# Optimization experiments

Measured on AMD Instinct MI355X. Metric: run time of the kernel, lower is better.

The kernel has to match this reference:

```python
import jax, jax.numpy as jnp
import numpy as np
from jax.ops import segment_sum

N_NODES = 100000
N_HEDGES = 20000
N_EDGES = 800000
N_TYPES = 2
IN_DIM = 64
HID = 64
OUT_DIM = 64


def setup_inputs() -> dict:
    key = jax.random.key(0)
    ks = jax.random.split(key, 16)
    inp = {
        "x": jax.random.normal(ks[0], (N_NODES, IN_DIM), jnp.float32),
        "h_prev": jax.random.normal(ks[1], (N_NODES, HID), jnp.float32),
        "node_idx": jax.random.randint(ks[2], (N_EDGES,), 0, N_NODES),
        "hedge_idx": jax.random.randint(ks[3], (N_EDGES,), 0, N_HEDGES),
        "edge_attr": jax.random.randint(ks[4], (N_EDGES,), 0, N_TYPES),
        "W_conv": jax.random.normal(ks[5], (N_TYPES, IN_DIM, HID), jnp.float32) * 0.05,
        "b_conv": jax.random.normal(ks[6], (N_TYPES, HID), jnp.float32) * 0.05,
        "W_mix": jax.random.normal(ks[7], (N_TYPES * HID, HID), jnp.float32) * 0.05,
        "b_mix": jax.random.normal(ks[8], (HID,), jnp.float32) * 0.05,
        "W_ih": jax.random.normal(ks[9], (HID, 3 * HID), jnp.float32) * 0.05,
        "W_hh": jax.random.normal(ks[10], (HID, 3 * HID), jnp.float32) * 0.05,
        "b_ih": jax.random.normal(ks[11], (3 * HID,), jnp.float32) * 0.05,
        "b_hh": jax.random.normal(ks[12], (3 * HID,), jnp.float32) * 0.05,
        "W_ro": jax.random.normal(ks[13], (HID, OUT_DIM), jnp.float32) * 0.05,
        "b_ro": jax.random.normal(ks[14], (OUT_DIM,), jnp.float32) * 0.05,
    }
    return inp


def _hypergraph_conv(x, node_idx, hedge_idx, mask, W, b):
    # PyG HypergraphConv (no attention): out = D^{-1} H B^{-1} H^T (x W) + b,
    # restricted to incidences where mask==1 (per edge type).
    xl = x @ W  # [N, hid]
    D = segment_sum(mask, node_idx, num_segments=N_NODES)       # node degree
    B = segment_sum(mask, hedge_idx, num_segments=N_HEDGES)     # hyperedge degree
    Dinv = jnp.where(D > 0, 1.0 / D, 0.0)
    Binv = jnp.where(B > 0, 1.0 / B, 0.0)
    # node -> hyperedge aggregation, scaled by B^{-1}
    ef = segment_sum(mask[:, None] * xl[node_idx], hedge_idx, num_segments=N_HEDGES)
    ef = ef * Binv[:, None]
    # hyperedge -> node aggregation, scaled by D^{-1}
    no = segment_sum(mask[:, None] * ef[hedge_idx], node_idx, num_segments=N_NODES)
    no = no * Dinv[:, None]
    return no + b


def reference(x, h_prev, node_idx, hedge_idx, edge_attr,
              W_conv, b_conv, W_mix, b_mix,
              W_ih, W_hh, b_ih, b_hh, W_ro, b_ro):
    outs = []
    for t in range(N_TYPES):
        mask = (edge_attr == t).astype(x.dtype)
        outs.append(_hypergraph_conv(x, node_idx, hedge_idx, mask, W_conv[t], b_conv[t]))
    h = jax.nn.relu(jnp.concatenate(outs, axis=1) @ W_mix + b_mix)  # [N, hid]
    # torch GRUCell: gates ordered (reset, update, new)
    gi = h @ W_ih + b_ih
    gh = h_prev @ W_hh + b_hh
    gi_r, gi_z, gi_n = jnp.split(gi, 3, axis=1)
    gh_r, gh_z, gh_n = jnp.split(gh, 3, axis=1)
    r = jax.nn.sigmoid(gi_r + gh_r)
    z = jax.nn.sigmoid(gi_z + gh_z)
    n = jnp.tanh(gi_n + r * gh_n)
    h_next = (1.0 - z) * n + z * h_prev
    out = (h_next @ W_ro + b_ro)[:, :3]
    return (h_next, out)
```

## Files before the change

kernel.cpp:

```cpp
#include <hip/hip_runtime.h>
#include <hip/hip_bf16.h>

#define N_NODES 100000
#define N_HEDGES 20000
#define N_EDGES 800000
#define HSEG (2 * N_HEDGES)
#define NSEG (2 * N_NODES)
#define MSEG (HSEG + NSEG)

#define EPB 4096
#define NBLK_A ((N_EDGES + EPB - 1) / EPB)
#define NHB 313
#define NBUCK 704
#define TOTB (NBUCK * NBLK_A)
#define SCANB ((TOTB + 2047) / 2048)
#define RKCAP 8192

#define CAST_BLOCKS (N_NODES * 64 / 8 / 256)
#define PACK_BLOCKS 16

#define MIX_PK  (4 * 4 * 64 * 8)
#define GRU_PK  (2 * 2 * 12 * 64 * 8)

typedef __hip_bfloat16 bf16;
typedef __attribute__((ext_vector_type(8))) short bf16x8;
typedef __attribute__((ext_vector_type(4))) float f32x4;

__device__ __forceinline__ bf16 f2b(float v) { return __float2bfloat16(v); }
__device__ __forceinline__ short f2s(float v) {
    bf16 b = __float2bfloat16(v);
    return *reinterpret_cast<short*>(&b);
}
__device__ __forceinline__ uint pk2(float a, float b) {
    return (uint)(unsigned short)f2s(a) | ((uint)(unsigned short)f2s(b) << 16);
}
__device__ __forceinline__ bf16x8 pack8(float4 a, float4 b) {
    bf16x8 r = {f2s(a.x), f2s(a.y), f2s(a.z), f2s(a.w),
                f2s(b.x), f2s(b.y), f2s(b.z), f2s(b.w)};
    return r;
}
__device__ __forceinline__ float fast_sigmoid(float x) {
    return __builtin_amdgcn_rcpf(1.f + __expf(-x));
}
__device__ __forceinline__ float fast_tanh(float x) {
    return 1.f - 2.f * __builtin_amdgcn_rcpf(1.f + __expf(2.f * x));
}

__global__ __launch_bounds__(256) void k_front(
    const int* __restrict__ node_idx, const int* __restrict__ hedge_idx,
    const int* __restrict__ attr, uint* __restrict__ rk12,
    int* __restrict__ bcnt,
    const float* __restrict__ x, bf16* __restrict__ xb,
    const float* __restrict__ Wc, const float* __restrict__ Wm,
    const float* __restrict__ bc_g, const float* __restrict__ bm,
    const float* __restrict__ Wih, const float* __restrict__ Whh,
    bf16* __restrict__ gru_pk, bf16* __restrict__ mixf_pk,
    float* __restrict__ bfused) {
    __shared__ int bc[NBUCK];
    int b = blockIdx.x;
    int tid = threadIdx.x;
    if (b < NBLK_A) {
        for (int i = tid; i < NBUCK; i += 256) bc[i] = 0;
        __syncthreads();
        int e0 = b * EPB;
        for (int it = 0; it < EPB / 256; ++it) {
            int e = e0 + it * 256 + tid;
            if (e < N_EDGES) {
                int t = attr[e];
                int s1 = t * N_HEDGES + hedge_idx[e];
                int s2 = HSEG + t * N_NODES + node_idx[e];
                int b1 = s1 >> 7;
                int b2 = NHB + ((s2 - HSEG) >> 9);
                int r1 = atomicAdd(&bc[b1], 1);
                int r2 = atomicAdd(&bc[b2], 1);
                rk12[e] = (uint)(r1 & 0xFFFF) | ((uint)r2 << 16);
            }
        }
        __syncthreads();
        for (int i = tid; i < NBUCK; i += 256) bcnt[i * NBLK_A + b] = bc[i];
    } else if (b < NBLK_A + CAST_BLOCKS) {
        size_t i = ((size_t)(b - NBLK_A) * 256 + tid) * 8;
        const float* xp = x + i;
        float4 a = *(const float4*)xp;
        float4 bb = *(const float4*)(xp + 4);
        *(bf16x8*)(xb + i) = pack8(a, bb);
    } else {
        int idx = (b - NBLK_A - CAST_BLOCKS) * 256 + tid;
        int stride = PACK_BLOCKS * 256;
        for (int i = idx; i < GRU_PK; i += stride) {
            int j = i & 7;
            int r = i >> 3;
            int ln = r & 63;
            int r2i = r >> 6;
            int ct = r2i % 12;
            int r3 = r2i / 12;
            int kt = r3 & 1;
            int mat = r3 >> 1;
            int k = kt * 32 + ((ln >> 4) << 3) + j;
            int n = ct * 16 + (ln & 15);
            float v = mat == 0 ? Wih[k * 192 + n] : Whh[k * 192 + n];
            gru_pk[i] = f2b(v);
        }
        for (int i = idx; i < MIX_PK; i += stride) {
            int j = i & 7, ln = (i >> 3) & 63, r2i = i >> 9;
            int ct = r2i & 3, kt = r2i >> 2;
            int k = kt * 32 + ((ln >> 4) << 3) + j;
            int n = ct * 16 + (ln & 15);
            int t = k >> 6, kk = k & 63;
            float s = 0.f;
            for (int q = 0; q < 64; ++q)
                s += Wc[((size_t)t * 64 + kk) * 64 + q] * Wm[(size_t)(t * 64 + q) * 64 + n];
            mixf_pk[i] = f2b(s);
        }
        for (int i = idx; i < 64; i += stride) {
            float s = bm[i];
            for (int q = 0; q < 64; ++q)
                s += bc_g[q] * Wm[(size_t)q * 64 + i] + bc_g[64 + q] * Wm[(size_t)(64 + q) * 64 + i];
            bfused[i] = s;
        }
    }
}

__global__ __launch_bounds__(256) void k_scan1(const int* __restrict__ cnt,
                                               int* __restrict__ off,
                                               int* __restrict__ bsum) {
    __shared__ int s[256];
    int base = blockIdx.x * 2048 + threadIdx.x * 8;
    int v[8];
    int tsum = 0;
#pragma unroll
    for (int j = 0; j < 8; ++j) {
        int g = base + j;
        v[j] = (g < TOTB) ? cnt[g] : 0;
        tsum += v[j];
    }
    s[threadIdx.x] = tsum;
    __syncthreads();
    for (int o = 1; o < 256; o <<= 1) {
        int t = (threadIdx.x >= o) ? s[threadIdx.x - o] : 0;
        __syncthreads();
        s[threadIdx.x] += t;
        __syncthreads();
    }
    int run = s[threadIdx.x] - tsum;
#pragma unroll
    for (int j = 0; j < 8; ++j) {
        int g = base + j;
        if (g < TOTB) off[g] = run;
        run += v[j];
    }
    if (threadIdx.x == 255) bsum[blockIdx.x] = s[255];
}

__global__ __launch_bounds__(1024) void k_scan2(int* __restrict__ bsum) {
    __shared__ int s[1024];
    int tid = threadIdx.x;
    int v = (tid < SCANB) ? bsum[tid] : 0;
    s[tid] = v;
    __syncthreads();
    for (int o = 1; o < 1024; o <<= 1) {
        int t = (tid >= o) ? s[tid - o] : 0;
        __syncthreads();
        s[tid] += t;
        __syncthreads();
    }
    if (tid < SCANB) bsum[tid] = s[tid] - v;
}

__global__ __launch_bounds__(256) void k_scan3(int* __restrict__ off,
                                               const int* __restrict__ bsum) {
    int base = blockIdx.x * 2048 + threadIdx.x * 8;
    int add = bsum[blockIdx.x];
#pragma unroll
    for (int j = 0; j < 8; ++j) {
        int g = base + j;
        if (g < TOTB) off[g] += add;
    }
    if (blockIdx.x == 0 && threadIdx.x == 0) off[TOTB] = 2 * N_EDGES;
}

__global__ __launch_bounds__(256) void k_bscatter(const int* __restrict__ node_idx,
                                                  const int* __restrict__ hedge_idx,
                                                  const int* __restrict__ attr,
                                                  const uint* __restrict__ rk12,
                                                  const int* __restrict__ bbase,
                                                  int2* __restrict__ pairs) {
    int b = blockIdx.x, tid = threadIdx.x;
    int e0 = b * EPB;
    for (int it = 0; it < EPB / 256; ++it) {
        int e = e0 + it * 256 + tid;
        if (e < N_EDGES) {
            int t = attr[e], n = node_idx[e], h = hedge_idx[e];
            int s1 = t * N_HEDGES + h;
            int s2 = HSEG + t * N_NODES + n;
            int b1 = s1 >> 7;
            int b2 = NHB + ((s2 - HSEG) >> 9);
            uint rk = rk12[e];
            int p1 = bbase[b1 * NBLK_A + b] + (int)(rk & 0xFFFF);
            int p2 = bbase[b2 * NBLK_A + b] + (int)(rk >> 16);
            pairs[p1] = make_int2(s1, n);
            pairs[p2] = make_int2(s2, t * N_HEDGES + h);
        }
    }
}

__global__ __launch_bounds__(256) void k_bfinal(const int* __restrict__ bbase,
                                                const int2* __restrict__ pairs,
                                                int* __restrict__ off,
                                                int* __restrict__ sortedAll) {
    __shared__ int scnt[512];
    __shared__ int exs[512];
    __shared__ int ssum[256];
    __shared__ unsigned short rk[RKCAP];
    int bucket = blockIdx.x, tid = threadIdx.x;
    int seg_first, nseg;
    if (bucket < NHB) {
        seg_first = bucket << 7;
        nseg = min(128, HSEG - seg_first);
    } else {
        int bi = bucket - NHB;
        seg_first = HSEG + (bi << 9);
        nseg = min(512, MSEG - seg_first);
    }
    int bstart = bbase[bucket * NBLK_A];
    int bend = bbase[(bucket + 1) * NBLK_A];
    for (int i = tid; i < 512; i += 256) scnt[i] = 0;
    __syncthreads();
    for (int i = bstart + tid; i < bend; i += 256) {
        int li = i - bstart;
        int key = pairs[i].x;
        int r = atomicAdd(&scnt[key - seg_first], 1);
        if (li < RKCAP) rk[li] = (unsigned short)r;
    }
    __syncthreads();
    int a0 = (2 * tid < nseg) ? scnt[2 * tid] : 0;
    int a1 = (2 * tid + 1 < nseg) ? scnt[2 * tid + 1] : 0;
    ssum[tid] = a0 + a1;
    __syncthreads();
    for (int o = 1; o < 256; o <<= 1) {
        int t = (tid >= o) ? ssum[tid - o] : 0;
        __syncthreads();
        ssum[tid] += t;
        __syncthreads();
    }
    int pb = ssum[tid] - (a0 + a1);
    exs[2 * tid] = pb;
    exs[2 * tid + 1] = pb + a0;
    if (2 * tid < nseg) off[seg_first + 2 * tid] = bstart + pb;
    if (2 * tid + 1 < nseg) off[seg_first + 2 * tid + 1] = bstart + pb + a0;
    if (bucket == NBUCK - 1 && tid == 0) off[MSEG] = 2 * N_EDGES;
    __syncthreads();
    for (int i = bstart + tid; i < bend; i += 256) {
        int li = i - bstart;
        if (li < RKCAP) {
            int2 pr = pairs[i];
            int pos = bstart + exs[pr.x - seg_first] + (int)rk[li];
            sortedAll[pos] = pr.y;
        }
    }
}

__device__ __forceinline__ void seg_gather(const int* __restrict__ off,
                                           const int* __restrict__ sortedAll,
                                           const bf16* __restrict__ rows,
                                           int seg0, int lane,
                                           float acc[8], int* total) {
    int q = lane >> 4, l16 = lane & 15;
    int ov = 0;
    if (lane < 5) ov = off[seg0 + lane];
    int myb = __shfl(ov, q);
    int mye = __shfl(ov, q + 1);
#pragma unroll
    for (int j = 0; j < 8; ++j) acc[j] = 0.f;
    int cb = (l16 & 7) * 8;
    int i = myb + (l16 >> 3);
    for (; i + 2 < mye; i += 4) {
        int idx0 = sortedAll[i];
        int idx1 = sortedAll[i + 2];
        uint4 v0 = *(const uint4*)(rows + (size_t)idx0 * 64 + cb);
        uint4 v1 = *(const uint4*)(rows + (size_t)idx1 * 64 + cb);
        acc[0] += __uint_as_float(v0.x << 16);
        acc[1] += __uint_as_float(v0.x & 0xffff0000u);
        acc[2] += __uint_as_float(v0.y << 16);
        acc[3] += __uint_as_float(v0.y & 0xffff0000u);
        acc[4] += __uint_as_float(v0.z << 16);
        acc[5] += __uint_as_float(v0.z & 0xffff0000u);
        acc[6] += __uint_as_float(v0.w << 16);
        acc[7] += __uint_as_float(v0.w & 0xffff0000u);
        acc[0] += __uint_as_float(v1.x << 16);
        acc[1] += __uint_as_float(v1.x & 0xffff0000u);
        acc[2] += __uint_as_float(v1.y << 16);
        acc[3] += __uint_as_float(v1.y & 0xffff0000u);
        acc[4] += __uint_as_float(v1.z << 16);
        acc[5] += __uint_as_float(v1.z & 0xffff0000u);
        acc[6] += __uint_as_float(v1.w << 16);
        acc[7] += __uint_as_float(v1.w & 0xffff0000u);
    }
    if (i < mye) {
        int idx = sortedAll[i];
        uint4 v = *(const uint4*)(rows + (size_t)idx * 64 + cb);
        acc[0] += __uint_as_float(v.x << 16);
        acc[1] += __uint_as_float(v.x & 0xffff0000u);
        acc[2] += __uint_as_float(v.y << 16);
        acc[3] += __uint_as_float(v.y & 0xffff0000u);
        acc[4] += __uint_as_float(v.z << 16);
        acc[5] += __uint_as_float(v.z & 0xffff0000u);
        acc[6] += __uint_as_float(v.w << 16);
        acc[7] += __uint_as_float(v.w & 0xffff0000u);
    }
#pragma unroll
    for (int j = 0; j < 8; ++j) acc[j] += __shfl_xor(acc[j], 8);
    *total = mye - myb;
}

__global__ __launch_bounds__(256) void k_ef2(const int* __restrict__ off,
                                             const int* __restrict__ sortedAll,
                                             const bf16* __restrict__ xb,
                                             bf16* __restrict__ ef16) {
    int wid = threadIdx.x >> 6, lane = threadIdx.x & 63;
    int seg0 = (blockIdx.x * 4 + wid) * 4;
    if (seg0 >= HSEG) return;
    float acc[8];
    int tot;
    seg_gather(off, sortedAll, xb, seg0, lane, acc, &tot);
    float scale = tot > 0 ? 1.0f / (float)tot : 0.f;
    int q = lane >> 4, l16 = lane & 15;
    if (l16 < 8) {
        int s = seg0 + q;
        uint4 w;
        w.x = pk2(acc[0] * scale, acc[1] * scale);
        w.y = pk2(acc[2] * scale, acc[3] * scale);
        w.z = pk2(acc[4] * scale, acc[5] * scale);
        w.w = pk2(acc[6] * scale, acc[7] * scale);
        *(uint4*)(ef16 + (size_t)s * 64 + l16 * 8) = w;
    }
}

__global__ __launch_bounds__(256) void k_no2(const int* __restrict__ off,
                                             const int* __restrict__ sortedAll,
                                             const bf16* __restrict__ ef16,
                                             bf16* __restrict__ agg16) {
    int wid = threadIdx.x >> 6, lane = threadIdx.x & 63;
    int j0 = (blockIdx.x * 4 + wid) * 4;
    if (j0 >= NSEG) return;
    float acc[8];
    int tot;
    seg_gather(off, sortedAll, ef16, HSEG + j0, lane, acc, &tot);
    float scale = tot > 0 ? 1.0f / (float)tot : 0.f;
    int q = lane >> 4, l16 = lane & 15;
    if (l16 < 8) {
        int j = j0 + q;
        uint4 w;
        w.x = pk2(acc[0] * scale, acc[1] * scale);
        w.y = pk2(acc[2] * scale, acc[3] * scale);
        w.z = pk2(acc[4] * scale, acc[5] * scale);
        w.w = pk2(acc[6] * scale, acc[7] * scale);
        *(uint4*)(agg16 + (size_t)j * 64 + l16 * 8) = w;
    }
}

#define GRU_TILES (N_NODES / 16)
__global__ __launch_bounds__(512) void k_mixgru(const bf16* __restrict__ gru_pk,
                                                const bf16* __restrict__ mixf_pk,
                                                const float* __restrict__ bfused,
                                                const bf16* __restrict__ agg16,
                                                const float* __restrict__ h_prev,
                                                const float* __restrict__ bih_g,
                                                const float* __restrict__ bhh_g,
                                                const float* __restrict__ Wro_g,
                                                const float* __restrict__ bro_g,
                                                float* __restrict__ out_h,
                                                float* __restrict__ out_o) {
    __shared__ __align__(16) bf16 Wpk[GRU_PK];
    __shared__ __align__(16) bf16 Wmx[MIX_PK];
    __shared__ __align__(16) bf16 bounce[8 * 1024];
    {
        const bf16x8* src = (const bf16x8*)gru_pk;
        bf16x8* dst = (bf16x8*)Wpk;
        for (int i = threadIdx.x; i < GRU_PK / 8; i += 512) dst[i] = src[i];
        const bf16x8* src2 = (const bf16x8*)mixf_pk;
        bf16x8* dst2 = (bf16x8*)Wmx;
        for (int i = threadIdx.x; i < MIX_PK / 8; i += 512) dst2[i] = src2[i];
    }
    __syncthreads();

    int wid = threadIdx.x >> 6, lane = threadIdx.x & 63;
    int quad = lane >> 4, l16 = lane & 15;
    bf16* bnc = &bounce[wid * 1024];

    float bmv[4];
#pragma unroll
    for (int ct = 0; ct < 4; ++ct) bmv[ct] = bfused[ct * 16 + l16];

    float br_c[4], bz_c[4], bin_c[4], bhn_c[4], wv[4][3];
#pragma unroll
    for (int cc = 0; cc < 4; ++cc) {
        int col = cc * 16 + l16;
        br_c[cc] = bih_g[col] + bhh_g[col];
        bz_c[cc] = bih_g[64 + col] + bhh_g[64 + col];
        bin_c[cc] = bih_g[128 + col];
        bhn_c[cc] = bhh_g[128 + col];
        wv[cc][0] = Wro_g[col * 64 + 0];
        wv[cc][1] = Wro_g[col * 64 + 1];
        wv[cc][2] = Wro_g[col * 64 + 2];
    }
    float bro0 = bro_g[0], bro1 = bro_g[1], bro2 = bro_g[2];

    int wave = blockIdx.x * 8 + wid;
    int n_waves = gridDim.x * 8;

    for (int tile = wave; tile < GRU_TILES; tile += n_waves) {
        int row0 = tile * 16;
        int arow = row0 + l16;

        bf16x8 af[4];
#pragma unroll
        for (int kt = 0; kt < 4; ++kt) {
            const bf16* src = (kt < 2)
                ? agg16 + (size_t)arow * 64 + kt * 32 + quad * 8
                : agg16 + ((size_t)N_NODES + arow) * 64 + (kt - 2) * 32 + quad * 8;
            af[kt] = *(const bf16x8*)src;
        }
#define LDBM(kt, ct) (*(const bf16x8*)&Wmx[(((kt)*4 + (ct)) * 64 + lane) * 8])
#pragma unroll
        for (int ct = 0; ct < 4; ++ct) {
            f32x4 acc = {bmv[ct], bmv[ct], bmv[ct], bmv[ct]};
#pragma unroll
            for (int kt = 0; kt < 4; ++kt)
                acc = __builtin_amdgcn_mfma_f32_16x16x32_bf16(af[kt], LDBM(kt, ct), acc, 0, 0, 0);
#pragma unroll
            for (int rg = 0; rg < 4; ++rg) {
                int r = quad * 4 + rg;
                int chunk = ct * 2 + (l16 >> 3);
                int cs = chunk ^ (r & 7);
                bnc[r * 64 + cs * 8 + (l16 & 7)] = f2b(fmaxf(acc[rg], 0.f));
            }
        }
#undef LDBM
        asm volatile("s_waitcnt lgkmcnt(0)" ::: "memory");
        __builtin_amdgcn_sched_barrier(0);

        bf16x8 ha0 = *(const bf16x8*)&bnc[l16 * 64 + (quad ^ (l16 & 7)) * 8];
        bf16x8 ha1 = *(const bf16x8*)&bnc[l16 * 64 + ((quad + 4) ^ (l16 & 7)) * 8];

        const float* pp = h_prev + (size_t)arow * 64 + quad * 8;
        bf16x8 pa0 = pack8(*(const float4*)pp, *(const float4*)(pp + 4));
        bf16x8 pa1 = pack8(*(const float4*)(pp + 32), *(const float4*)(pp + 36));

        float p[4][3];
#pragma unroll
        for (int rg = 0; rg < 4; ++rg) p[rg][0] = p[rg][1] = p[rg][2] = 0.f;

#pragma unroll
        for (int cc = 0; cc < 4; ++cc) {
#define LDB(mat, kt, ct) (*(const bf16x8*)&Wpk[((((mat)*2 + (kt)) * 12 + (ct)) * 64 + lane) * 8])
            f32x4 rs = {br_c[cc], br_c[cc], br_c[cc], br_c[cc]};
            f32x4 zs = {bz_c[cc], bz_c[cc], bz_c[cc], bz_c[cc]};
            f32x4 gin = {bin_c[cc], bin_c[cc], bin_c[cc], bin_c[cc]};
            f32x4 ghn = {bhn_c[cc], bhn_c[cc], bhn_c[cc], bhn_c[cc]};
            rs = __builtin_amdgcn_mfma_f32_16x16x32_bf16(ha0, LDB(0, 0, cc), rs, 0, 0, 0);
            rs = __builtin_amdgcn_mfma_f32_16x16x32_bf16(ha1, LDB(0, 1, cc), rs, 0, 0, 0);
            rs = __builtin_amdgcn_mfma_f32_16x16x32_bf16(pa0, LDB(1, 0, cc), rs, 0, 0, 0);
            rs = __builtin_amdgcn_mfma_f32_16x16x32_bf16(pa1, LDB(1, 1, cc), rs, 0, 0, 0);
            zs = __builtin_amdgcn_mfma_f32_16x16x32_bf16(ha0, LDB(0, 0, cc + 4), zs, 0, 0, 0);
            zs = __builtin_amdgcn_mfma_f32_16x16x32_bf16(ha1, LDB(0, 1, cc + 4), zs, 0, 0, 0);
            zs = __builtin_amdgcn_mfma_f32_16x16x32_bf16(pa0, LDB(1, 0, cc + 4), zs, 0, 0, 0);
            zs = __builtin_amdgcn_mfma_f32_16x16x32_bf16(pa1, LDB(1, 1, cc + 4), zs, 0, 0, 0);
            gin = __builtin_amdgcn_mfma_f32_16x16x32_bf16(ha0, LDB(0, 0, cc + 8), gin, 0, 0, 0);
            gin = __builtin_amdgcn_mfma_f32_16x16x32_bf16(ha1, LDB(0, 1, cc + 8), gin, 0, 0, 0);
            ghn = __builtin_amdgcn_mfma_f32_16x16x32_bf16(pa0, LDB(1, 0, cc + 8), ghn, 0, 0, 0);
            ghn = __builtin_amdgcn_mfma_f32_16x16x32_bf16(pa1, LDB(1, 1, cc + 8), ghn, 0, 0, 0);
#undef LDB
#pragma unroll
            for (int rg = 0; rg < 4; ++rg) {
                int row = row0 + quad * 4 + rg;
                float pv = h_prev[(size_t)row * 64 + cc * 16 + l16];
                float rr = fast_sigmoid(rs[rg]);
                float zz = fast_sigmoid(zs[rg]);
                float nn = fast_tanh(gin[rg] + rr * ghn[rg]);
                float hn = (1.f - zz) * nn + zz * pv;
                out_h[(size_t)row * 64 + cc * 16 + l16] = hn;
                p[rg][0] += hn * wv[cc][0];
                p[rg][1] += hn * wv[cc][1];
                p[rg][2] += hn * wv[cc][2];
            }
        }
#pragma unroll
        for (int rg = 0; rg < 4; ++rg) {
#pragma unroll
            for (int m = 1; m < 16; m <<= 1) {
                p[rg][0] += __shfl_xor(p[rg][0], m);
                p[rg][1] += __shfl_xor(p[rg][1], m);
                p[rg][2] += __shfl_xor(p[rg][2], m);
            }
        }
        if (l16 == 0) {
#pragma unroll
            for (int rg = 0; rg < 4; ++rg) {
                int row = row0 + quad * 4 + rg;
                out_o[(size_t)row * 3 + 0] = p[rg][0] + bro0;
                out_o[(size_t)row * 3 + 1] = p[rg][1] + bro1;
                out_o[(size_t)row * 3 + 2] = p[rg][2] + bro2;
            }
        }
    }
}

extern "C" void kernel_launch(void* const* d_in, const int* in_sizes, int n_in,
                              void* d_out, int out_size, void* d_ws, size_t ws_size,
                              hipStream_t stream) {
    const float* x        = (const float*)d_in[0];
    const float* h_prev   = (const float*)d_in[1];
    const int* node_idx   = (const int*)d_in[2];
    const int* hedge_idx  = (const int*)d_in[3];
    const int* edge_attr  = (const int*)d_in[4];
    const float* W_conv   = (const float*)d_in[5];
    const float* b_conv   = (const float*)d_in[6];
    const float* W_mix    = (const float*)d_in[7];
    const float* b_mix    = (const float*)d_in[8];
    const float* W_ih     = (const float*)d_in[9];
    const float* W_hh     = (const float*)d_in[10];
    const float* b_ih     = (const float*)d_in[11];
    const float* b_hh     = (const float*)d_in[12];
    const float* W_ro     = (const float*)d_in[13];
    const float* b_ro     = (const float*)d_in[14];

    char* p = (char*)d_ws;
    auto alloc = [&](size_t bytes) {
        char* r = p;
        p += (bytes + 63) & ~(size_t)63;
        return r;
    };
    char* regA     = alloc((size_t)2 * N_NODES * 64 * 2);
    int2* pairs    = (int2*)regA;
    uint* rk12     = (uint*)(pairs + 2 * N_EDGES);
    int* bcnt      = (int*)(rk12 + N_EDGES);
    int* bsum      = bcnt + TOTB + 1;
    bf16* agg16    = (bf16*)regA;
    int* off       = (int*)alloc((size_t)(MSEG + 1) * 4);
    int* sortedAll = (int*)alloc((size_t)2 * N_EDGES * 4);
    bf16* xb       = (bf16*)alloc((size_t)N_NODES * 64 * 2);
    bf16* ef16     = (bf16*)alloc((size_t)HSEG * 64 * 2);
    bf16* gru_pk   = (bf16*)alloc((size_t)GRU_PK * 2);
    bf16* mixf_pk  = (bf16*)alloc((size_t)MIX_PK * 2);
    float* bfused  = (float*)alloc(64 * 4);

    float* out_h = (float*)d_out;
    float* out_o = out_h + (size_t)N_NODES * 64;

    k_front<<<NBLK_A + CAST_BLOCKS + PACK_BLOCKS, 256, 0, stream>>>(
        node_idx, hedge_idx, edge_attr, rk12, bcnt, x, xb,
        W_conv, W_mix, b_conv, b_mix, W_ih, W_hh, gru_pk, mixf_pk, bfused);
    k_scan1<<<SCANB, 256, 0, stream>>>(bcnt, bcnt, bsum);
    k_scan2<<<1, 1024, 0, stream>>>(bsum);
    k_scan3<<<SCANB, 256, 0, stream>>>(bcnt, bsum);
    k_bscatter<<<NBLK_A, 256, 0, stream>>>(node_idx, hedge_idx, edge_attr,
                                           rk12, bcnt, pairs);
    k_bfinal<<<NBUCK, 256, 0, stream>>>(bcnt, pairs, off, sortedAll);
    k_ef2<<<HSEG / 16, 256, 0, stream>>>(off, sortedAll, xb, ef16);
    k_no2<<<NSEG / 16, 256, 0, stream>>>(off, sortedAll, ef16, agg16);
    k_mixgru<<<512, 512, 0, stream>>>(gru_pk, mixf_pk, bfused, agg16, h_prev,
                                      b_ih, b_hh, W_ro, b_ro, out_h, out_o);
}
```

Before: 253.8 us.

## Apply mix weights per hyperedge before scatter and merge both edge types per node

The per-type W_mix slice is moved through the linear aggregation: each hyperedge feature row is multiplied by its type's mix weight block via MFMA in the hyperedge kernel. The node kernel then gathers both types for a node, scales and sums them, and adds bias and ReLU, writing a single 64-wide hidden buffer instead of two. The GRU kernel no longer does the mix GEMM and reads the precomputed hidden directly, and it launches one tile per wave instead of a persistent grid. This cuts node-side intermediate writes and reads by half and moves the mix matmul from 100k nodes onto 40k hyperedges, at the cost of an extra bf16 rounding at a different point.

Measured after the change: 319.5 us. +25.9%, slower.

```diff
diff --git a/kernel.cpp b/kernel.cpp
--- a/kernel.cpp
+++ b/kernel.cpp
@@ -260,20 +260,13 @@
     }
 }
 
-__device__ __forceinline__ void seg_gather(const int* __restrict__ off,
-                                           const int* __restrict__ sortedAll,
+__device__ __forceinline__ void run_gather(const int* __restrict__ sortedAll,
                                            const bf16* __restrict__ rows,
-                                           int seg0, int lane,
-                                           float acc[8], int* total) {
-    int q = lane >> 4, l16 = lane & 15;
-    int ov = 0;
-    if (lane < 5) ov = off[seg0 + lane];
-    int myb = __shfl(ov, q);
-    int mye = __shfl(ov, q + 1);
+                                           int myb, int mye, int i0, int cb,
+                                           float acc[8]) {
 #pragma unroll
     for (int j = 0; j < 8; ++j) acc[j] = 0.f;
-    int cb = (l16 & 7) * 8;
-    int i = myb + (l16 >> 3);
+    int i = myb + i0;
     for (; i + 2 < mye; i += 4) {
         int idx0 = sortedAll[i];
         int idx1 = sortedAll[i + 2];
@@ -308,89 +301,117 @@
         acc[6] += __uint_as_float(v.w << 16);
         acc[7] += __uint_as_float(v.w & 0xffff0000u);
     }
+}
+
+__global__ __launch_bounds__(256) void k_ef2w(const int* __restrict__ off,
+                                              const int* __restrict__ sortedAll,
+                                              const bf16* __restrict__ xb,
+                                              const bf16* __restrict__ mixf_pk,
+                                              bf16* __restrict__ eg16) {
+    __shared__ __align__(16) bf16 Wl[2 * 4 * 64 * 8];
+    __shared__ __align__(16) bf16 tile[16 * 64];
+    int seg0b = blockIdx.x * 16;
+    int t = (seg0b >= N_HEDGES) ? 1 : 0;
+    {
+        const bf16x8* src = (const bf16x8*)(mixf_pk + t * 4096);
+        bf16x8* dst = (bf16x8*)Wl;
+        for (int i = threadIdx.x; i < 4096 / 8; i += 256) dst[i] = src[i];
+    }
+    int wid = threadIdx.x >> 6, lane = threadIdx.x & 63;
+    int q = lane >> 4, l16 = lane & 15;
+
+    int seg0 = seg0b + wid * 4;
+    int ov = 0;
+    if (lane < 5) ov = off[seg0 + lane];
+    int myb = __shfl(ov, q);
+    int mye = __shfl(ov, q + 1);
+    float acc[8];
+    run_gather(sortedAll, xb, myb, mye, l16 >> 3, (l16 & 7) * 8, acc);
 #pragma unroll
     for (int j = 0; j < 8; ++j) acc[j] += __shfl_xor(acc[j], 8);
-    *total = mye - myb;
-}
-
-__global__ __launch_bounds__(256) void k_ef2(const int* __restrict__ off,
-                                             const int* __restrict__ sortedAll,
-                                             const bf16* __restrict__ xb,
-                                             bf16* __restrict__ ef16) {
-    int wid = threadIdx.x >> 6, lane = threadIdx.x & 63;
-    int seg0 = (blockIdx.x * 4 + wid) * 4;
-    if (seg0 >= HSEG) return;
-    float acc[8];
-    int tot;
-    seg_gather(off, sortedAll, xb, seg0, lane, acc, &tot);
-    float scale = tot > 0 ? 1.0f / (float)tot : 0.f;
-    int q = lane >> 4, l16 = lane & 15;
+    float scale = (mye > myb) ? 1.0f / (float)(mye - myb) : 0.f;
+    int r = wid * 4 + q;
     if (l16 < 8) {
-        int s = seg0 + q;
+        int cs = l16 ^ (r & 7);
         uint4 w;
         w.x = pk2(acc[0] * scale, acc[1] * scale);
         w.y = pk2(acc[2] * scale, acc[3] * scale);
         w.z = pk2(acc[4] * scale, acc[5] * scale);
         w.w = pk2(acc[6] * scale, acc[7] * scale);
-        *(uint4*)(ef16 + (size_t)s * 64 + l16 * 8) = w;
-    }
-}
-
-__global__ __launch_bounds__(256) void k_no2(const int* __restrict__ off,
-                                             const int* __restrict__ sortedAll,
-                                             const bf16* __restrict__ ef16,
-                                             bf16* __restrict__ agg16) {
+        *(uint4*)&tile[r * 64 + cs * 8] = w;
+    }
+    __syncthreads();
+
+    bf16x8 a0 = *(const bf16x8*)&tile[l16 * 64 + (q ^ (l16 & 7)) * 8];
+    bf16x8 a1 = *(const bf16x8*)&tile[l16 * 64 + ((q + 4) ^ (l16 & 7)) * 8];
+    const f32x4 zero = {0.f, 0.f, 0.f, 0.f};
+#define LDW(ktl) (*(const bf16x8*)&Wl[(((ktl)*4 + wid) * 64 + lane) * 8])
+    f32x4 d = __builtin_amdgcn_mfma_f32_16x16x32_bf16(a0, LDW(0), zero, 0, 0, 0);
+    d = __builtin_amdgcn_mfma_f32_16x16x32_bf16(a1, LDW(1), d, 0, 0, 0);
+#undef LDW
+#pragma unroll
+    for (int rg = 0; rg < 4; ++rg)
+        eg16[(size_t)(seg0b + q * 4 + rg) * 64 + wid * 16 + l16] = f2b(d[rg]);
+}
+
+__global__ __launch_bounds__(256) void k_no2h(const int* __restrict__ off,
+                                              const int* __restrict__ sortedAll,
+                                              const bf16* __restrict__ eg16,
+                                              const float* __restrict__ bfused,
+                                              bf16* __restrict__ hbuf16) {
     int wid = threadIdx.x >> 6, lane = threadIdx.x & 63;
-    int j0 = (blockIdx.x * 4 + wid) * 4;
-    if (j0 >= NSEG) return;
-    float acc[8];
-    int tot;
-    seg_gather(off, sortedAll, ef16, HSEG + j0, lane, acc, &tot);
-    float scale = tot > 0 ? 1.0f / (float)tot : 0.f;
+    int n0 = (blockIdx.x * 4 + wid) * 4;
+    if (n0 >= N_NODES) return;
     int q = lane >> 4, l16 = lane & 15;
+    int cb = (l16 & 7) * 8, i0 = l16 >> 3;
+    int ov = 0;
+    if (lane < 5) ov = off[HSEG + n0 + lane];
+    else if (lane >= 8 && lane < 13) ov = off[HSEG + N_NODES + n0 + (lane - 8)];
+    int b0 = __shfl(ov, q), e0 = __shfl(ov, q + 1);
+    int b1 = __shfl(ov, 8 + q), e1 = __shfl(ov, 9 + q);
+    float a0[8], a1[8];
+    run_gather(sortedAll, eg16, b0, e0, i0, cb, a0);
+    run_gather(sortedAll, eg16, b1, e1, i0, cb, a1);
+    float s0 = (e0 > b0) ? 1.0f / (float)(e0 - b0) : 0.f;
+    float s1 = (e1 > b1) ? 1.0f / (float)(e1 - b1) : 0.f;
+    float v[8];
+#pragma unroll
+    for (int j = 0; j < 8; ++j) {
+        v[j] = a0[j] * s0 + a1[j] * s1;
+        v[j] += __shfl_xor(v[j], 8);
+    }
     if (l16 < 8) {
-        int j = j0 + q;
+#pragma unroll
+        for (int j = 0; j < 8; ++j) v[j] = fmaxf(v[j] + bfused[cb + j], 0.f);
         uint4 w;
-        w.x = pk2(acc[0] * scale, acc[1] * scale);
-        w.y = pk2(acc[2] * scale, acc[3] * scale);
-        w.z = pk2(acc[4] * scale, acc[5] * scale);
-        w.w = pk2(acc[6] * scale, acc[7] * scale);
-        *(uint4*)(agg16 + (size_t)j * 64 + l16 * 8) = w;
+        w.x = pk2(v[0], v[1]);
+        w.y = pk2(v[2], v[3]);
+        w.z = pk2(v[4], v[5]);
+        w.w = pk2(v[6], v[7]);
+        *(uint4*)(hbuf16 + (size_t)(n0 + q) * 64 + cb) = w;
     }
 }
 
 #define GRU_TILES (N_NODES / 16)
-__global__ __launch_bounds__(512) void k_mixgru(const bf16* __restrict__ gru_pk,
-                                                const bf16* __restrict__ mixf_pk,
-                                                const float* __restrict__ bfused,
-                                                const bf16* __restrict__ agg16,
-                                                const float* __restrict__ h_prev,
-                                                const float* __restrict__ bih_g,
-                                                const float* __restrict__ bhh_g,
-                                                const float* __restrict__ Wro_g,
-                                                const float* __restrict__ bro_g,
-                                                float* __restrict__ out_h,
-                                                float* __restrict__ out_o) {
+__global__ __launch_bounds__(512) void k_gru(const bf16* __restrict__ gru_pk,
+                                             const bf16* __restrict__ hbuf16,
+                                             const float* __restrict__ h_prev,
+                                             const float* __restrict__ bih_g,
+                                             const float* __restrict__ bhh_g,
+                                             const float* __restrict__ Wro_g,
+                                             const float* __restrict__ bro_g,
+                                             float* __restrict__ out_h,
+                                             float* __restrict__ out_o) {
     __shared__ __align__(16) bf16 Wpk[GRU_PK];
-    __shared__ __align__(16) bf16 Wmx[MIX_PK];
-    __shared__ __align__(16) bf16 bounce[8 * 1024];
     {
         const bf16x8* src = (const bf16x8*)gru_pk;
         bf16x8* dst = (bf16x8*)Wpk;
         for (int i = threadIdx.x; i < GRU_PK / 8; i += 512) dst[i] = src[i];
-        const bf16x8* src2 = (const bf16x8*)mixf_pk;
-        bf16x8* dst2 = (bf16x8*)Wmx;
-        for (int i = threadIdx.x; i < MIX_PK / 8; i += 512) dst2[i] = src2[i];
     }
     __syncthreads();
 
     int wid = threadIdx.x >> 6, lane = threadIdx.x & 63;
     int quad = lane >> 4, l16 = lane & 15;
-    bf16* bnc = &bounce[wid * 1024];
-
-    float bmv[4];
-#pragma unroll
-    for (int ct = 0; ct < 4; ++ct) bmv[ct] = bfused[ct * 16 + l16];
 
     float br_c[4], bz_c[4], bin_c[4], bhn_c[4], wv[4][3];
 #pragma unroll
@@ -412,37 +433,9 @@
     for (int tile = wave; tile < GRU_TILES; tile += n_waves) {
         int row0 = tile * 16;
         int arow = row0 + l16;
-
-        bf16x8 af[4];
-#pragma unroll
-        for (int kt = 0; kt < 4; ++kt) {
-            const bf16* src = (kt < 2)
-                ? agg16 + (size_t)arow * 64 + kt * 32 + quad * 8
-                : agg16 + ((size_t)N_NODES + arow) * 64 + (kt - 2) * 32 + quad * 8;
-            af[kt] = *(const bf16x8*)src;
-        }
-#define LDBM(kt, ct) (*(const bf16x8*)&Wmx[(((kt)*4 + (ct)) * 64 + lane) * 8])
-#pragma unroll
-        for (int ct = 0; ct < 4; ++ct) {
-            f32x4 acc = {bmv[ct], bmv[ct], bmv[ct], bmv[ct]};
-#pragma unroll
-            for (int kt = 0; kt < 4; ++kt)
-                acc = __builtin_amdgcn_mfma_f32_16x16x32_bf16(af[kt], LDBM(kt, ct), acc, 0, 0, 0);
-#pragma unroll
-            for (int rg = 0; rg < 4; ++rg) {
-                int r = quad * 4 + rg;
-                int chunk = ct * 2 + (l16 >> 3);
-                int cs = chunk ^ (r & 7);
-                bnc[r * 64 + cs * 8 + (l16 & 7)] = f2b(fmaxf(acc[rg], 0.f));
-            }
-        }
-#undef LDBM
-        asm volatile("s_waitcnt lgkmcnt(0)" ::: "memory");
-        __builtin_amdgcn_sched_barrier(0);
-
-        bf16x8 ha0 = *(const bf16x8*)&bnc[l16 * 64 + (quad ^ (l16 & 7)) * 8];
-        bf16x8 ha1 = *(const bf16x8*)&bnc[l16 * 64 + ((quad + 4) ^ (l16 & 7)) * 8];
-
+        const bf16* ha_p = hbuf16 + (size_t)arow * 64 + quad * 8;
+        bf16x8 ha0 = *(const bf16x8*)ha_p;
+        bf16x8 ha1 = *(const bf16x8*)(ha_p + 32);
         const float* pp = h_prev + (size_t)arow * 64 + quad * 8;
         bf16x8 pa0 = pack8(*(const float4*)pp, *(const float4*)(pp + 4));
         bf16x8 pa1 = pack8(*(const float4*)(pp + 32), *(const float4*)(pp + 36));
@@ -536,11 +529,11 @@
     uint* rk12     = (uint*)(pairs + 2 * N_EDGES);
     int* bcnt      = (int*)(rk12 + N_EDGES);
     int* bsum      = bcnt + TOTB + 1;
-    bf16* agg16    = (bf16*)regA;
+    bf16* hbuf16   = (bf16*)regA;
     int* off       = (int*)alloc((size_t)(MSEG + 1) * 4);
     int* sortedAll = (int*)alloc((size_t)2 * N_EDGES * 4);
     bf16* xb       = (bf16*)alloc((size_t)N_NODES * 64 * 2);
-    bf16* ef16     = (bf16*)alloc((size_t)HSEG * 64 * 2);
+    bf16* eg16     = (bf16*)alloc((size_t)HSEG * 64 * 2);
     bf16* gru_pk   = (bf16*)alloc((size_t)GRU_PK * 2);
     bf16* mixf_pk  = (bf16*)alloc((size_t)MIX_PK * 2);
     float* bfused  = (float*)alloc(64 * 4);
@@ -557,8 +550,9 @@
     k_bscatter<<<NBLK_A, 256, 0, stream>>>(node_idx, hedge_idx, edge_attr,
                                            rk12, bcnt, pairs);
     k_bfinal<<<NBUCK, 256, 0, stream>>>(bcnt, pairs, off, sortedAll);
-    k_ef2<<<HSEG / 16, 256, 0, stream>>>(off, sortedAll, xb, ef16);
-    k_no2<<<NSEG / 16, 256, 0, stream>>>(off, sortedAll, ef16, agg16);
-    k_mixgru<<<512, 512, 0, stream>>>(gru_pk, mixf_pk, bfused, agg16, h_prev,
-                                      b_ih, b_hh, W_ro, b_ro, out_h, out_o);
-}
+    k_ef2w<<<HSEG / 16, 256, 0, stream>>>(off, sortedAll, xb, mixf_pk, eg16);
+    k_no2h<<<N_NODES / 16, 256, 0, stream>>>(off, sortedAll, eg16, bfused, hbuf16);
+    k_gru<<<(GRU_TILES + 7) / 8, 512, 0, stream>>>(gru_pk, hbuf16, h_prev,
+                                                   b_ih, b_hh, W_ro, b_ro,
+                                                   out_h, out_o);
+}
```
